# Optimization experiments

Hardware: AMD Instinct MI355X
Metric: run time of the kernel (lower is better)

The kernel has to match this reference:

```python
import jax, jax.numpy as jnp
import numpy as np

# Static model dims
B, N, EMB, D, H, HD, L, NC = 1, 4096, 1024, 512, 8, 64, 2, 2
# Per-head local neighborhood sizes (round(pi*local_k^2) in the original, static here)
K_PER_HEAD = (32, 48, 64, 80, 96, 112, 128, 160)
SCALE = float(np.sqrt(HD))  # sigma_sq = sqrt(head_dim) in the original


def _ln(x, g, b, eps=1e-5):
    m = x.mean(-1, keepdims=True)
    v = ((x - m) ** 2).mean(-1, keepdims=True)
    return (x - m) * jax.lax.rsqrt(v + eps) * g + b


def _gather(a, idx):
    # a: [B, N, ...], idx: [B, N, K] -> [B, N, K, ...] (per-batch row gather, as k_h[range(B), indices])
    return jax.vmap(lambda ah, ih: ah[ih])(a, idx)


def setup_inputs() -> dict:
    key = jax.random.key(0)
    ks = iter(jax.random.split(key, 48))
    w = lambda shape: 0.02 * jax.random.normal(next(ks), shape, jnp.float32)
    return {
        "x": jax.random.normal(next(ks), (B, N, EMB), jnp.float32),
        "distance": 10.0 * jax.random.uniform(next(ks), (B, N, N), jnp.float32),
        "indices": jax.random.randint(next(ks), (B, N, K_PER_HEAD[-1]), 0, N, jnp.int32),
        "row": jax.random.randint(next(ks), (B, N), 0, 128, jnp.int32),
        "col": jax.random.randint(next(ks), (B, N), 0, 128, jnp.int32),
        # adapter (ResidualFullyConnected, simplified: linear proj + 1 residual layer)
        "adapter_w": w((EMB, D)), "adapter_b": jnp.zeros((D,), jnp.float32),
        "res_w": w((D, D)), "res_b": jnp.zeros((D,), jnp.float32),
        # per-block params, stacked over depth L
        "ln1_g": jnp.ones((L, D), jnp.float32), "ln1_b": jnp.zeros((L, D), jnp.float32),
        "qkv_w": w((L, D, 3 * D)), "qkv_b": jnp.zeros((L, 3 * D), jnp.float32),
        "proj_w": w((L, D, D)), "proj_b": jnp.zeros((L, D), jnp.float32),
        "ln2_g": jnp.ones((L, D), jnp.float32), "ln2_b": jnp.zeros((L, D), jnp.float32),
        "fc1_w": w((L, D, 4 * D)), "fc1_b": jnp.zeros((L, 4 * D), jnp.float32),
        "fc2_w": w((L, 4 * D, D)), "fc2_b": jnp.zeros((L, D), jnp.float32),
        # per-head decay rate parameter (DecayNetwork lambda_p); reparam = softplus
        "lam": 0.5 + w((L, H)),
        "lnf_g": jnp.ones((D,), jnp.float32), "lnf_b": jnp.zeros((D,), jnp.float32),
        "head_w": w((D, NC)), "head_b": jnp.zeros((NC,), jnp.float32),
    }


def _forward(x, distance, indices, adapter_w, adapter_b, res_w, res_b,
             ln1_g, ln1_b, qkv_w, qkv_b, proj_w, proj_b,
             ln2_g, ln2_b, fc1_w, fc1_b, fc2_w, fc2_b,
             lam, lnf_g, lnf_b, head_w, head_b):
    h = x @ adapter_w + adapter_b
    h = h + jax.nn.relu(h @ res_w + res_b)  # residual adapter layer
    for l in range(L):
        # --- spatial multi-head attention with per-head KNN window + decay log-bias ---
        xa = _ln(h, ln1_g[l], ln1_b[l])
        qkv = (xa @ qkv_w[l] + qkv_b[l]).reshape(B, N, 3, H, HD).transpose(2, 0, 3, 1, 4)
        q, k, v = qkv[0], qkv[1], qkv[2]          # [B,H,N,d]
        qn = jnp.sum(q * q, -1)                    # [B,H,N]  |q|^2
        kn = jnp.sum(k * k, -1)                    # [B,H,N]  |k|^2
        heads = []
        for hh in range(H):
            Kh = K_PER_HEAD[hh]
            idx = indices[:, :, :Kh]               # [B,N,Kh] nearest neighbors
            ksel = _gather(k[:, hh], idx)          # [B,N,Kh,d]
            vsel = _gather(v[:, hh], idx)          # [B,N,Kh,d]
            knsel = _gather(kn[:, hh], idx)        # [B,N,Kh]
            attn = jnp.einsum('bnd,bnkd->bnk', q[:, hh], ksel) / SCALE
            attn = attn - 0.5 * (qn[:, hh][..., None] + knsel) / SCALE  # norm correction
            dsel = jnp.take_along_axis(distance, idx, axis=-1)          # [B,N,Kh]
            decay = jnp.exp(-jax.nn.softplus(lam[l, hh]) * dsel) + 1e-6
            attn = jax.nn.softmax(attn + jnp.log(decay), axis=-1)
            heads.append(jnp.einsum('bnk,bnkd->bnd', attn, vsel))
        xo = jnp.stack(heads, 2).reshape(B, N, D)  # [B,N,H,d] -> [B,N,D]
        h = h + (xo @ proj_w[l] + proj_b[l])
        # --- MLP ---
        xm = _ln(h, ln2_g[l], ln2_b[l])
        h = h + (jax.nn.gelu(xm @ fc1_w[l] + fc1_b[l]) @ fc2_w[l] + fc2_b[l])
    h = _ln(h, lnf_g, lnf_b, eps=1e-6)
    return h.mean(axis=1) @ head_w + head_b  # avg pool + head -> [B, num_classes]


def reference(x, distance, indices, row, col, adapter_w, adapter_b, res_w, res_b,
              ln1_g, ln1_b, qkv_w, qkv_b, proj_w, proj_b,
              ln2_g, ln2_b, fc1_w, fc1_b, fc2_w, fc2_b,
              lam, lnf_g, lnf_b, head_w, head_b):
    # row/col are carried as metadata in the original forward and unused by the math
    return _forward(x, distance, indices, adapter_w, adapter_b, res_w, res_b,
                    ln1_g, ln1_b, qkv_w, qkv_b, proj_w, proj_b,
                    ln2_g, ln2_b, fc1_w, fc1_b, fc2_w, fc2_b,
                    lam, lnf_g, lnf_b, head_w, head_b)
```

## Files before the change

### kernel.cpp

```cpp
#include <hip/hip_runtime.h>
#include <hip/hip_bf16.h>

#define NTOK 4096
#define EMB 1024
#define DMODEL 512
#define NHEAD 8
#define NLAYER 2
#define NCLS 2
#define KMAX 160

typedef __attribute__((ext_vector_type(8))) short bf16x8;
typedef __attribute__((ext_vector_type(4))) float f32x4;

__device__ inline unsigned short f2b(float f) {
    unsigned u = __float_as_uint(f);
    u = u + 0x7FFFu + ((u >> 16) & 1u);
    return (unsigned short)(u >> 16);
}
__device__ inline float b2f(unsigned short s) {
    return __uint_as_float((unsigned)s << 16);
}

__device__ inline float wsum(float v) {
    for (int o = 32; o > 0; o >>= 1) v += __shfl_xor(v, o, 64);
    return v;
}
__device__ inline float wmax(float v) {
    for (int o = 32; o > 0; o >>= 1) v = fmaxf(v, __shfl_xor(v, o, 64));
    return v;
}

typedef __attribute__((address_space(3))) unsigned lds_u32_t;
typedef __attribute__((address_space(1))) const unsigned glb_u32_t;
__device__ inline void gload16(const void* g, void* l) {
    __builtin_amdgcn_global_load_lds((glb_u32_t*)(unsigned long long)g,
                                     (lds_u32_t*)(unsigned)(unsigned long long)l,
                                     16, 0, 0);
}

__device__ const int g_s0cnt[8]  = {576, 448, 720, 144, 365, 490, 460, 159};
__device__ const int g_s0h[8]    = {7, 7, 6, 6, 5, 4, 3, 2};
__device__ const int g_s0base[8] = {0, 576, 160, 880, 659, 534, 564, 865};
__device__ const int g_s1cnt[8]  = {0, 160, 0, 659, 534, 564, 865, 1024};
__device__ const int g_s1h[8]    = {0, 6, 0, 5, 4, 3, 2, 1};
#define ATTN_BLOCKS (2207 * 8)

__global__ __launch_bounds__(256) void wcvt_k(const float* __restrict__ W,
                                              unsigned short* __restrict__ Wt,
                                              int K, int N)
{
    __shared__ unsigned short tile[64][72];
    size_t ls = (size_t)K * N * blockIdx.z;
    const float* Wl = W + ls;
    unsigned short* Wtl = Wt + ls;
    int k0 = blockIdx.x * 64, n0 = blockIdx.y * 64;
    int t = threadIdx.x;
    int kl = t >> 2, nb = (t & 3) * 16;
    const float* src = Wl + (size_t)(k0 + kl) * N + n0 + nb;
#pragma unroll
    for (int i = 0; i < 4; i++) {
        float4 v = *(const float4*)(src + 4 * i);
        tile[nb + 4 * i + 0][kl] = f2b(v.x);
        tile[nb + 4 * i + 1][kl] = f2b(v.y);
        tile[nb + 4 * i + 2][kl] = f2b(v.z);
        tile[nb + 4 * i + 3][kl] = f2b(v.w);
    }
    __syncthreads();
    int nl = t >> 2, ks = (t & 3) * 16;
    unsigned short* dst = Wtl + (size_t)(n0 + nl) * K + k0 + ks;
    *(uint4*)dst = *(const uint4*)&tile[nl][ks];
    *(uint4*)(dst + 8) = *(const uint4*)&tile[nl][ks + 8];
}

__global__ __launch_bounds__(256) void xcvt_k(const float* __restrict__ X,
                                              unsigned short* __restrict__ Xb)
{
    int i = (blockIdx.x * 256 + threadIdx.x) * 8;
    float4 a = *(const float4*)(X + i);
    float4 b = *(const float4*)(X + i + 4);
    unsigned short o[8];
    o[0] = f2b(a.x); o[1] = f2b(a.y); o[2] = f2b(a.z); o[3] = f2b(a.w);
    o[4] = f2b(b.x); o[5] = f2b(b.y); o[6] = f2b(b.z); o[7] = f2b(b.w);
    *(uint4*)(Xb + i) = *(const uint4*)o;
}

__global__ __launch_bounds__(256) void dsel_k(const float* __restrict__ distance,
                                              const int* __restrict__ indices,
                                              float* __restrict__ dsel)
{
    int n = blockIdx.x, t = threadIdx.x;
    if (t < KMAX) {
        int idx = indices[(size_t)n * KMAX + t];
        dsel[(size_t)n * KMAX + t] = distance[(size_t)n * NTOK + idx];
    }
}

template <int BM, int BN, int WM, int WN, int MODE>
__global__ __launch_bounds__(256) void mgemm_k(
    const unsigned short* __restrict__ A, const unsigned short* __restrict__ Wt,
    const float* __restrict__ bias, const float* __restrict__ resid,
    float* __restrict__ Cf, unsigned short* __restrict__ Cb,
    int M, int N, int K)
{
    constexpr int SM = BM / WM;
    constexpr int SN = BN / WN;
    constexpr int MR = SM / 16;
    constexpr int NR = SN / 16;

    __shared__ unsigned short Asl[BM * 32];
    __shared__ unsigned short Bsl[BN * 32];

    int tid = threadIdx.x;
    int bm = blockIdx.x * BM, bn = blockIdx.y * BN;
    int lane = tid & 63, wid = tid >> 6;
    int wm = wid / WN, wn = wid % WN;
    int l15 = lane & 15, l4 = lane >> 4;

    f32x4 acc[MR][NR] = {};

    int sr = tid >> 2, sc = (tid & 3) * 8;
    const unsigned short* Asrc = A  + (size_t)(bm + sr) * K + sc;
    const unsigned short* Bsrc = Wt + (size_t)(bn + sr) * K + sc;
    unsigned short* Adst = &Asl[sr * 32 + sc];
    unsigned short* Bdst = &Bsl[sr * 32 + sc];

    int arow0 = (wm * SM + l15) * 32 + l4 * 8;
    int brow0 = (wn * SN + l15) * 32 + l4 * 8;

    for (int k0 = 0; k0 < K; k0 += 32) {
#pragma unroll
        for (int i = 0; i < BM / 64; i++)
            gload16(Asrc + (size_t)(i * 64) * K + k0, Adst + i * 64 * 32);
#pragma unroll
        for (int i = 0; i < BN / 64; i++)
            gload16(Bsrc + (size_t)(i * 64) * K + k0, Bdst + i * 64 * 32);
        __syncthreads();

        bf16x8 af[MR], bfr[NR];
#pragma unroll
        for (int mr = 0; mr < MR; mr++) af[mr] = *(const bf16x8*)&Asl[arow0 + mr * 16 * 32];
#pragma unroll
        for (int nr = 0; nr < NR; nr++) bfr[nr] = *(const bf16x8*)&Bsl[brow0 + nr * 16 * 32];
#pragma unroll
        for (int mr = 0; mr < MR; mr++)
#pragma unroll
            for (int nr = 0; nr < NR; nr++)
                acc[mr][nr] = __builtin_amdgcn_mfma_f32_16x16x32_bf16(af[mr], bfr[nr], acc[mr][nr], 0, 0, 0);
        __syncthreads();
    }

#pragma unroll
    for (int mr = 0; mr < MR; mr++) {
#pragma unroll
        for (int nr = 0; nr < NR; nr++) {
            int col = bn + wn * SN + nr * 16 + l15;
            float bcol = bias[col];
#pragma unroll
            for (int r = 0; r < 4; r++) {
                int row = bm + wm * SM + mr * 16 + l4 * 4 + r;
                size_t off = (size_t)row * N + col;
                float v = acc[mr][nr][r] + bcol;
                if (MODE == 0) {
                    Cf[off] = v;
                } else if (MODE == 1) {
                    Cf[off] = resid[off] + fmaxf(v, 0.f);
                } else if (MODE == 2) {
                    float t3 = tanhf(0.7978845608028654f * (v + 0.044715f * v * v * v));
                    Cb[off] = f2b(0.5f * v * (1.f + t3));
                } else if (MODE == 3) {
                    Cf[off] = resid[off] + v;
                } else if (MODE == 4) {
                    Cf[off] = v;
                    Cb[off] = f2b(v);
                } else {
                    Cb[off] = f2b(v);
                }
            }
        }
    }
}

template <int OUTB>
__global__ __launch_bounds__(256) void ln_k(
    const float* __restrict__ X, const float* __restrict__ g,
    const float* __restrict__ bta, void* __restrict__ Yv, float eps)
{
    int row = blockIdx.x;
    int tid = threadIdx.x;
    const float* xr = X + (size_t)row * DMODEL;
    float v0 = xr[tid], v1 = xr[tid + 256];
    __shared__ float red[8];
    float s = wsum(v0 + v1);
    int wid = tid >> 6, lane = tid & 63;
    if (lane == 0) red[wid] = s;
    __syncthreads();
    float m = (red[0] + red[1] + red[2] + red[3]) * (1.f / DMODEL);
    float d0 = v0 - m, d1 = v1 - m;
    float sq = wsum(d0 * d0 + d1 * d1);
    if (lane == 0) red[4 + wid] = sq;
    __syncthreads();
    float var = (red[4] + red[5] + red[6] + red[7]) * (1.f / DMODEL);
    float rs = 1.0f / sqrtf(var + eps);
    float y0 = d0 * rs * g[tid] + bta[tid];
    float y1 = d1 * rs * g[tid + 256] + bta[tid + 256];
    if (OUTB) {
        unsigned short* Y = (unsigned short*)Yv;
        Y[(size_t)row * DMODEL + tid] = f2b(y0);
        Y[(size_t)row * DMODEL + tid + 256] = f2b(y1);
    } else {
        float* Y = (float*)Yv;
        Y[(size_t)row * DMODEL + tid] = y0;
        Y[(size_t)row * DMODEL + tid + 256] = y1;
    }
}

__global__ __launch_bounds__(256) void attn_k(
    const unsigned short* __restrict__ qkv,
    const int* __restrict__ indices, const float* __restrict__ dsel,
    const float* __restrict__ lam, unsigned short* __restrict__ xo, int layer)
{
    int xcd = blockIdx.x & 7;
    int t = blockIdx.x >> 3;
    int hh, blk;
    int c0 = g_s0cnt[xcd];
    if (t < c0) {
        hh = g_s0h[xcd]; blk = g_s0base[xcd] + t;
    } else {
        t -= c0;
        int c1 = g_s1cnt[xcd];
        if (t < c1) {
            hh = g_s1h[xcd]; blk = t;
        } else if (xcd == 7 && t - c1 < 1024) {
            hh = 0; blk = t - c1;
        } else {
            return;
        }
    }

    int wid = threadIdx.x >> 6, lane = threadIdx.x & 63;
    int n = blk * 4 + wid;
    int Kh = 32 + 16 * hh + (hh == 7 ? 16 : 0);

    __shared__ __align__(16) float qs[4][64];
    __shared__ float asc[4][KMAX];
    __shared__ int   sidx[4][KMAX];

    float qd = b2f(qkv[(size_t)n * 1536 + hh * 64 + lane]);
    qs[wid][lane] = qd;
    float qn2 = wsum(qd * qd);
    float sp = log1pf(expf(lam[layer * NHEAD + hh]));

    const int* irow = indices + (size_t)n * KMAX;
    const float* drow = dsel + (size_t)n * KMAX;

    int sub = lane & 3, grp = lane >> 2;
    float qv[16];
#pragma unroll
    for (int c = 0; c < 2; c++) {
        float4 ta = *(const float4*)&qs[wid][c * 32 + sub * 8];
        float4 tb = *(const float4*)&qs[wid][c * 32 + sub * 8 + 4];
        qv[c * 8 + 0] = ta.x; qv[c * 8 + 1] = ta.y; qv[c * 8 + 2] = ta.z; qv[c * 8 + 3] = ta.w;
        qv[c * 8 + 4] = tb.x; qv[c * 8 + 5] = tb.y; qv[c * 8 + 6] = tb.z; qv[c * 8 + 7] = tb.w;
    }

    int iters = Kh >> 4;
    for (int it = 0; it < iters; it++) {
        int kk = it * 16 + grp;
        int idx = irow[kk];
        const uint4* krow = (const uint4*)(qkv + (size_t)idx * 1536 + 512 + hh * 64);
        uint4 ka = krow[sub];
        uint4 kb = krow[4 + sub];
        unsigned kw[8];
        *(uint4*)&kw[0] = ka;
        *(uint4*)&kw[4] = kb;
        float dp = 0.f, knp = 0.f;
#pragma unroll
        for (int w = 0; w < 8; w++) {
            float lo = __uint_as_float(kw[w] << 16);
            float hi = __uint_as_float(kw[w] & 0xFFFF0000u);
            dp += qv[2 * w] * lo + qv[2 * w + 1] * hi;
            knp += lo * lo + hi * hi;
        }
        dp += __shfl_xor(dp, 1, 64);
        dp += __shfl_xor(dp, 2, 64);
        knp += __shfl_xor(knp, 1, 64);
        knp += __shfl_xor(knp, 2, 64);
        float dd = drow[kk];
        float dec = expf(-sp * dd) + 1e-6f;
        float s = (dp - 0.5f * (qn2 + knp)) * 0.125f + logf(dec);
        if (sub == 0) {
            asc[wid][kk] = s;
            sidx[wid][kk] = idx;
        }
    }

    float s0 = (lane < Kh) ? asc[wid][lane] : -1e30f;
    float s1 = (lane + 64 < Kh) ? asc[wid][lane + 64] : -1e30f;
    float s2 = (lane + 128 < Kh) ? asc[wid][lane + 128] : -1e30f;
    float mx = wmax(fmaxf(fmaxf(s0, s1), s2));
    float e0 = (s0 > -1e29f) ? expf(s0 - mx) : 0.f;
    float e1 = (s1 > -1e29f) ? expf(s1 - mx) : 0.f;
    float e2 = (s2 > -1e29f) ? expf(s2 - mx) : 0.f;
    float se = wsum(e0 + e1 + e2);
    float inv = 1.f / se;
    if (lane < Kh)       asc[wid][lane]       = e0 * inv;
    if (lane + 64 < Kh)  asc[wid][lane + 64]  = e1 * inv;
    if (lane + 128 < Kh) asc[wid][lane + 128] = e2 * inv;

    int g = lane >> 3, q = lane & 7;
    const uint4* vb = (const uint4*)(qkv + 1024 + hh * 64 + q * 8);
    float a8[8] = {};
    int k0 = 0;
    int kmain = Kh & ~31;
    for (; k0 < kmain; k0 += 32) {
        int ii[4]; float aa[4]; uint4 vv[4];
#pragma unroll
        for (int u = 0; u < 4; u++) {
            int kk = k0 + u * 8 + g;
            ii[u] = sidx[wid][kk];
            aa[u] = asc[wid][kk];
        }
#pragma unroll
        for (int u = 0; u < 4; u++) vv[u] = vb[(size_t)ii[u] * 192];
#pragma unroll
        for (int u = 0; u < 4; u++) {
            const unsigned short* vp = (const unsigned short*)&vv[u];
#pragma unroll
            for (int d = 0; d < 8; d++) a8[d] += aa[u] * b2f(vp[d]);
        }
    }
    if (Kh & 16) {
        int ii[2]; float aa[2]; uint4 vv[2];
#pragma unroll
        for (int u = 0; u < 2; u++) {
            int kk = k0 + u * 8 + g;
            ii[u] = sidx[wid][kk];
            aa[u] = asc[wid][kk];
        }
#pragma unroll
        for (int u = 0; u < 2; u++) vv[u] = vb[(size_t)ii[u] * 192];
#pragma unroll
        for (int u = 0; u < 2; u++) {
            const unsigned short* vp = (const unsigned short*)&vv[u];
#pragma unroll
            for (int d = 0; d < 8; d++) a8[d] += aa[u] * b2f(vp[d]);
        }
    }
#pragma unroll
    for (int d = 0; d < 8; d++) {
        a8[d] += __shfl_xor(a8[d], 8, 64);
        a8[d] += __shfl_xor(a8[d], 16, 64);
        a8[d] += __shfl_xor(a8[d], 32, 64);
    }
    if (lane < 8) {
        unsigned o[4];
#pragma unroll
        for (int p = 0; p < 4; p++)
            o[p] = ((unsigned)f2b(a8[2 * p + 1]) << 16) | (unsigned)f2b(a8[2 * p]);
        *(uint4*)(xo + (size_t)n * DMODEL + hh * 64 + lane * 8) = *(uint4*)o;
    }
}

__global__ __launch_bounds__(512) void colpart_k(const float* __restrict__ Y, float* __restrict__ part)
{
    int c = threadIdx.x;
    int blk = blockIdx.x;
    const float* p = Y + (size_t)blk * 16 * DMODEL + c;
    float s = 0.f;
#pragma unroll
    for (int r = 0; r < 16; r++) s += p[r * DMODEL];
    part[blk * DMODEL + c] = s;
}

__global__ __launch_bounds__(512) void finhead_k(
    const float* __restrict__ part, const float* __restrict__ head_w,
    const float* __restrict__ head_b, float* __restrict__ out)
{
    __shared__ float mv[DMODEL];
    int c = threadIdx.x;
    float s = 0.f;
    for (int i = 0; i < 256; i++) s += part[i * DMODEL + c];
    mv[c] = s * (1.f / NTOK);
    __syncthreads();
    if (c < 64) {
        float a0 = 0.f, a1 = 0.f;
        for (int d = c; d < DMODEL; d += 64) {
            float m = mv[d];
            a0 += m * head_w[d * NCLS + 0];
            a1 += m * head_w[d * NCLS + 1];
        }
        a0 = wsum(a0);
        a1 = wsum(a1);
        if (c == 0) { out[0] = a0 + head_b[0]; out[1] = a1 + head_b[1]; }
    }
}

extern "C" void kernel_launch(void* const* d_in, const int* in_sizes, int n_in,
                              void* d_out, int out_size, void* d_ws, size_t ws_size,
                              hipStream_t stream)
{
    const float* x        = (const float*)d_in[0];
    const float* distance = (const float*)d_in[1];
    const int*   indices  = (const int*)d_in[2];
    const float* adapter_w = (const float*)d_in[5];
    const float* adapter_b = (const float*)d_in[6];
    const float* res_w     = (const float*)d_in[7];
    const float* res_b     = (const float*)d_in[8];
    const float* ln1_g     = (const float*)d_in[9];
    const float* ln1_b     = (const float*)d_in[10];
    const float* qkv_w     = (const float*)d_in[11];
    const float* qkv_b     = (const float*)d_in[12];
    const float* proj_w    = (const float*)d_in[13];
    const float* proj_b    = (const float*)d_in[14];
    const float* ln2_g     = (const float*)d_in[15];
    const float* ln2_b     = (const float*)d_in[16];
    const float* fc1_w     = (const float*)d_in[17];
    const float* fc1_b     = (const float*)d_in[18];
    const float* fc2_w     = (const float*)d_in[19];
    const float* fc2_b     = (const float*)d_in[20];
    const float* lam       = (const float*)d_in[21];
    const float* lnf_g     = (const float*)d_in[22];
    const float* lnf_b     = (const float*)d_in[23];
    const float* head_w    = (const float*)d_in[24];
    const float* head_b    = (const float*)d_in[25];
    float* out = (float*)d_out;

    char* wsb = (char*)d_ws;
    float* h   = (float*)(wsb);
    float* h0  = (float*)(wsb + (8u << 20));
    float* dsel = (float*)(wsb + (8u << 20));
    char* shared = wsb + (16u << 20);
    unsigned short* xb    = (unsigned short*)shared;
    unsigned short* qkvbb = (unsigned short*)shared;
    unsigned short* fc1b  = (unsigned short*)shared;
    unsigned short* adapter_wt = (unsigned short*)(shared + (8u << 20));
    unsigned short* res_wt     = (unsigned short*)(shared + (9u << 20));
    unsigned short* lnb  = (unsigned short*)(wsb + (40u << 20));
    unsigned short* h0b  = lnb;
    unsigned short* xob  = (unsigned short*)(wsb + (44u << 20));
    unsigned short* qkv_wt = (unsigned short*)(wsb + (48u << 20));
    unsigned short* proj_wt = (unsigned short*)(wsb + (51u << 20));
    unsigned short* fc1_wt  = (unsigned short*)(wsb + (52u << 20));
    unsigned short* fc2_wt  = (unsigned short*)(wsb + (56u << 20));
    float* part = (float*)(wsb + (60u << 20));

    dim3 blk(256);

    xcvt_k<<<(NTOK * EMB) / 2048, blk, 0, stream>>>(x, xb);
    wcvt_k<<<dim3(EMB / 64, DMODEL / 64, 1), blk, 0, stream>>>(adapter_w, adapter_wt, EMB, DMODEL);
    wcvt_k<<<dim3(DMODEL / 64, DMODEL / 64, 1), blk, 0, stream>>>(res_w, res_wt, DMODEL, DMODEL);
    wcvt_k<<<dim3(DMODEL / 64, 1536 / 64, NLAYER), blk, 0, stream>>>(qkv_w, qkv_wt, DMODEL, 1536);
    wcvt_k<<<dim3(DMODEL / 64, DMODEL / 64, NLAYER), blk, 0, stream>>>(proj_w, proj_wt, DMODEL, DMODEL);
    wcvt_k<<<dim3(DMODEL / 64, 2048 / 64, NLAYER), blk, 0, stream>>>(fc1_w, fc1_wt, DMODEL, 2048);
    wcvt_k<<<dim3(2048 / 64, DMODEL / 64, NLAYER), blk, 0, stream>>>(fc2_w, fc2_wt, 2048, DMODEL);

    mgemm_k<64, 64, 2, 2, 4><<<dim3(NTOK / 64, DMODEL / 64), blk, 0, stream>>>(
        xb, adapter_wt, adapter_b, nullptr, h0, h0b, NTOK, DMODEL, EMB);
    mgemm_k<64, 64, 2, 2, 1><<<dim3(NTOK / 64, DMODEL / 64), blk, 0, stream>>>(
        h0b, res_wt, res_b, h0, h, nullptr, NTOK, DMODEL, DMODEL);

    dsel_k<<<NTOK, blk, 0, stream>>>(distance, indices, dsel);

    for (int l = 0; l < NLAYER; l++) {
        ln_k<1><<<NTOK, blk, 0, stream>>>(h, ln1_g + l * DMODEL, ln1_b + l * DMODEL, lnb, 1e-5f);
        mgemm_k<64, 128, 2, 2, 5><<<dim3(NTOK / 64, 1536 / 128), blk, 0, stream>>>(
            lnb, qkv_wt + (size_t)l * 1536 * DMODEL, qkv_b + l * 1536, nullptr,
            nullptr, qkvbb, NTOK, 1536, DMODEL);
        attn_k<<<ATTN_BLOCKS, blk, 0, stream>>>(qkvbb, indices, dsel, lam, xob, l);
        mgemm_k<64, 64, 2, 2, 3><<<dim3(NTOK / 64, DMODEL / 64), blk, 0, stream>>>(
            xob, proj_wt + (size_t)l * DMODEL * DMODEL, proj_b + l * DMODEL, h,
            h, nullptr, NTOK, DMODEL, DMODEL);
        ln_k<1><<<NTOK, blk, 0, stream>>>(h, ln2_g + l * DMODEL, ln2_b + l * DMODEL, lnb, 1e-5f);
        mgemm_k<64, 128, 2, 2, 2><<<dim3(NTOK / 64, 2048 / 128), blk, 0, stream>>>(
            lnb, fc1_wt + (size_t)l * 2048 * DMODEL, fc1_b + l * 2048, nullptr,
            nullptr, fc1b, NTOK, 2048, DMODEL);
        mgemm_k<64, 64, 2, 2, 3><<<dim3(NTOK / 64, DMODEL / 64), blk, 0, stream>>>(
            fc1b, fc2_wt + (size_t)l * DMODEL * 2048, fc2_b + l * DMODEL, h,
            h, nullptr, NTOK, DMODEL, 2048);
    }

    ln_k<0><<<NTOK, blk, 0, stream>>>(h, lnf_g, lnf_b, h0, 1e-6f);
    colpart_k<<<256, 512, 0, stream>>>(h0, part);
    finhead_k<<<1, 512, 0, stream>>>(part, head_w, head_b, out);
}
```

Before: 385.3 us.

## Double-buffer and swizzle GEMM LDS tiles; precompute key norms for attention

The MFMA GEMM now double-buffers its LDS tiles, prefetching the next K slice while computing the current one, which drops one barrier per iteration. An XOR swizzle on the global source column is meant to reduce LDS bank conflicts. Separately, the squared norm of each key per head is computed once per token in a new small kernel, so the attention kernel no longer recomputes it for every gathered neighbor, and the decay/log work moves into a per-lane pass after the dot products. This adds a kernel launch and doubles GEMM shared memory use, which can lower occupancy.

```diff
diff --git a/kernel.cpp b/kernel.cpp
--- a/kernel.cpp
+++ b/kernel.cpp
@@ -95,6 +95,16 @@
     }
 }
 
+__global__ __launch_bounds__(512) void knb_k(const unsigned short* __restrict__ qkv,
+                                             float* __restrict__ kn)
+{
+    int n = blockIdx.x;
+    int hh = threadIdx.x >> 6, lane = threadIdx.x & 63;
+    float kv = b2f(qkv[(size_t)n * 1536 + 512 + hh * 64 + lane]);
+    float ks = wsum(kv * kv);
+    if (lane == 0) kn[n * NHEAD + hh] = ks;
+}
+
 template <int BM, int BN, int WM, int WN, int MODE>
 __global__ __launch_bounds__(256) void mgemm_k(
     const unsigned short* __restrict__ A, const unsigned short* __restrict__ Wt,
@@ -107,8 +117,8 @@
     constexpr int MR = SM / 16;
     constexpr int NR = SN / 16;
 
-    __shared__ unsigned short Asl[BM * 32];
-    __shared__ unsigned short Bsl[BN * 32];
+    __shared__ unsigned short Asl[2][BM * 32];
+    __shared__ unsigned short Bsl[2][BN * 32];
 
     int tid = threadIdx.x;
     int bm = blockIdx.x * BM, bn = blockIdx.y * BN;
@@ -118,35 +128,44 @@
 
     f32x4 acc[MR][NR] = {};
 
-    int sr = tid >> 2, sc = (tid & 3) * 8;
-    const unsigned short* Asrc = A  + (size_t)(bm + sr) * K + sc;
-    const unsigned short* Bsrc = Wt + (size_t)(bn + sr) * K + sc;
-    unsigned short* Adst = &Asl[sr * 32 + sc];
-    unsigned short* Bdst = &Bsl[sr * 32 + sc];
-
-    int arow0 = (wm * SM + l15) * 32 + l4 * 8;
-    int brow0 = (wn * SN + l15) * 32 + l4 * 8;
-
-    for (int k0 = 0; k0 < K; k0 += 32) {
+    int sr = tid >> 2;
+    int scl = (((tid & 3) ^ ((sr >> 1) & 3))) * 8;
+    int dst_off = sr * 32 + (tid & 3) * 8;
+    const unsigned short* Asrc = A  + (size_t)(bm + sr) * K + scl;
+    const unsigned short* Bsrc = Wt + (size_t)(bn + sr) * K + scl;
+
+    int arow = wm * SM + l15;
+    int brow = wn * SN + l15;
+    int aoff0 = arow * 32 + (l4 ^ ((arow >> 1) & 3)) * 8;
+    int boff0 = brow * 32 + (l4 ^ ((brow >> 1) & 3)) * 8;
+
+    auto stage = [&](int buf, int k0) {
 #pragma unroll
         for (int i = 0; i < BM / 64; i++)
-            gload16(Asrc + (size_t)(i * 64) * K + k0, Adst + i * 64 * 32);
+            gload16(Asrc + (size_t)(i * 64) * K + k0, &Asl[buf][i * 64 * 32 + dst_off]);
 #pragma unroll
         for (int i = 0; i < BN / 64; i++)
-            gload16(Bsrc + (size_t)(i * 64) * K + k0, Bdst + i * 64 * 32);
-        __syncthreads();
-
+            gload16(Bsrc + (size_t)(i * 64) * K + k0, &Bsl[buf][i * 64 * 32 + dst_off]);
+    };
+
+    int nt = K / 32;
+    stage(0, 0);
+    __syncthreads();
+    int cur = 0;
+    for (int t = 0; t < nt; t++) {
+        if (t + 1 < nt) stage(cur ^ 1, (t + 1) * 32);
         bf16x8 af[MR], bfr[NR];
 #pragma unroll
-        for (int mr = 0; mr < MR; mr++) af[mr] = *(const bf16x8*)&Asl[arow0 + mr * 16 * 32];
-#pragma unroll
-        for (int nr = 0; nr < NR; nr++) bfr[nr] = *(const bf16x8*)&Bsl[brow0 + nr * 16 * 32];
+        for (int mr = 0; mr < MR; mr++) af[mr] = *(const bf16x8*)&Asl[cur][aoff0 + mr * 16 * 32];
+#pragma unroll
+        for (int nr = 0; nr < NR; nr++) bfr[nr] = *(const bf16x8*)&Bsl[cur][boff0 + nr * 16 * 32];
 #pragma unroll
         for (int mr = 0; mr < MR; mr++)
 #pragma unroll
             for (int nr = 0; nr < NR; nr++)
                 acc[mr][nr] = __builtin_amdgcn_mfma_f32_16x16x32_bf16(af[mr], bfr[nr], acc[mr][nr], 0, 0, 0);
         __syncthreads();
+        cur ^= 1;
     }
 
 #pragma unroll
@@ -216,6 +235,7 @@
 
 __global__ __launch_bounds__(256) void attn_k(
     const unsigned short* __restrict__ qkv,
+    const float* __restrict__ kn,
     const int* __restrict__ indices, const float* __restrict__ dsel,
     const float* __restrict__ lam, unsigned short* __restrict__ xo, int layer)
 {
@@ -273,30 +293,45 @@
         unsigned kw[8];
         *(uint4*)&kw[0] = ka;
         *(uint4*)&kw[4] = kb;
-        float dp = 0.f, knp = 0.f;
+        float dp = 0.f;
 #pragma unroll
         for (int w = 0; w < 8; w++) {
             float lo = __uint_as_float(kw[w] << 16);
             float hi = __uint_as_float(kw[w] & 0xFFFF0000u);
             dp += qv[2 * w] * lo + qv[2 * w + 1] * hi;
-            knp += lo * lo + hi * hi;
         }
         dp += __shfl_xor(dp, 1, 64);
         dp += __shfl_xor(dp, 2, 64);
-        knp += __shfl_xor(knp, 1, 64);
-        knp += __shfl_xor(knp, 2, 64);
-        float dd = drow[kk];
-        float dec = expf(-sp * dd) + 1e-6f;
-        float s = (dp - 0.5f * (qn2 + knp)) * 0.125f + logf(dec);
         if (sub == 0) {
-            asc[wid][kk] = s;
+            asc[wid][kk] = dp;
             sidx[wid][kk] = idx;
         }
     }
 
-    float s0 = (lane < Kh) ? asc[wid][lane] : -1e30f;
-    float s1 = (lane + 64 < Kh) ? asc[wid][lane + 64] : -1e30f;
-    float s2 = (lane + 128 < Kh) ? asc[wid][lane + 128] : -1e30f;
+    float s0 = -1e30f, s1 = -1e30f, s2 = -1e30f;
+    {
+        int kk = lane;
+        if (kk < Kh) {
+            float dp = asc[wid][kk];
+            float knv = kn[sidx[wid][kk] * NHEAD + hh];
+            float dec = expf(-sp * drow[kk]) + 1e-6f;
+            s0 = (dp - 0.5f * (qn2 + knv)) * 0.125f + logf(dec);
+        }
+        kk = lane + 64;
+        if (kk < Kh) {
+            float dp = asc[wid][kk];
+            float knv = kn[sidx[wid][kk] * NHEAD + hh];
+            float dec = expf(-sp * drow[kk]) + 1e-6f;
+            s1 = (dp - 0.5f * (qn2 + knv)) * 0.125f + logf(dec);
+        }
+        kk = lane + 128;
+        if (kk < Kh) {
+            float dp = asc[wid][kk];
+            float knv = kn[sidx[wid][kk] * NHEAD + hh];
+            float dec = expf(-sp * drow[kk]) + 1e-6f;
+            s2 = (dp - 0.5f * (qn2 + knv)) * 0.125f + logf(dec);
+        }
+    }
     float mx = wmax(fmaxf(fmaxf(s0, s1), s2));
     float e0 = (s0 > -1e29f) ? expf(s0 - mx) : 0.f;
     float e1 = (s1 > -1e29f) ? expf(s1 - mx) : 0.f;
@@ -442,7 +477,8 @@
     unsigned short* proj_wt = (unsigned short*)(wsb + (51u << 20));
     unsigned short* fc1_wt  = (unsigned short*)(wsb + (52u << 20));
     unsigned short* fc2_wt  = (unsigned short*)(wsb + (56u << 20));
-    float* part = (float*)(wsb + (60u << 20));
+    float* kn   = (float*)(wsb + (60u << 20));
+    float* part = (float*)(wsb + (60u << 20) + (1u << 18));
 
     dim3 blk(256);
 
@@ -466,7 +502,8 @@
         mgemm_k<64, 128, 2, 2, 5><<<dim3(NTOK / 64, 1536 / 128), blk, 0, stream>>>(
             lnb, qkv_wt + (size_t)l * 1536 * DMODEL, qkv_b + l * 1536, nullptr,
             nullptr, qkvbb, NTOK, 1536, DMODEL);
-        attn_k<<<ATTN_BLOCKS, blk, 0, stream>>>(qkvbb, indices, dsel, lam, xob, l);
+        knb_k<<<NTOK, 512, 0, stream>>>(qkvbb, kn);
+        attn_k<<<ATTN_BLOCKS, blk, 0, stream>>>(qkvbb, kn, indices, dsel, lam, xob, l);
         mgemm_k<64, 64, 2, 2, 3><<<dim3(NTOK / 64, DMODEL / 64), blk, 0, stream>>>(
             xob, proj_wt + (size_t)l * DMODEL * DMODEL, proj_b + l * DMODEL, h,
             h, nullptr, NTOK, DMODEL, DMODEL);
```

Measured after the change: 368.7 us. 1.05x faster.
